# Kernel tuning notes

Hardware: AMD Instinct MI355X
Metric: run time of the kernel (lower is better)

Reference implementation:

```python
import jax, jax.numpy as jnp
import numpy as np

D_MODEL = 1024
N_HEADS = 16
HEAD_DIM = D_MODEL // N_HEADS
D_LATENT = 256
LAMBDA_DECAY = 0.01
TIME_STEP = 0.01  # get_timestamps spacing; wall-clock base cancels in diffs
CLAMP = 1e4


def setup_inputs() -> dict:
    key = jax.random.key(0)
    ks = jax.random.split(key, 8)
    B, S = 2, 2048
    def w(k, i, o):
        return jax.random.normal(k, (i, o), dtype=jnp.float32) * 0.02
    return {
        "x": jax.random.normal(ks[0], (B, S, D_MODEL), dtype=jnp.float32),
        "Wq": w(ks[1], D_MODEL, D_MODEL),
        "Wk": w(ks[2], D_MODEL, D_MODEL),
        "Wv": w(ks[3], D_MODEL, D_MODEL),
        "Wo": w(ks[4], D_MODEL, D_MODEL),
        "W_down_kv": w(ks[5], D_MODEL, D_LATENT),
        "W_up_k": w(ks[6], D_LATENT, D_MODEL),
        "W_up_v": w(ks[7], D_LATENT, D_MODEL),
    }


def reference(x, Wq, Wk, Wv, Wo, W_down_kv, W_up_k, W_up_v):
    B, S, _ = x.shape
    q = x @ Wq
    k = x @ Wk
    v = x @ Wv
    latent_kv = (k + v) @ W_down_kv            # [B,S,d_latent]
    k_rec = latent_kv @ W_up_k                 # [B,S,d_model]
    v_rec = latent_kv @ W_up_v
    # split heads -> [B,H,S,hd]
    def heads(t):
        return t.reshape(B, S, N_HEADS, HEAD_DIM).transpose(0, 2, 1, 3)
    qh, kh, vh = heads(q), heads(k_rec), heads(v_rec)
    scale = 1.0 / (jnp.sqrt(jnp.float32(D_MODEL)) + 1e-8)
    scores = jnp.einsum("bhqd,bhkd->bhqk", qh, kh) * scale
    scores = jnp.clip(jnp.nan_to_num(scores, nan=-1e9), -CLAMP, CLAMP)
    # time decay: |t_i - t_j| = TIME_STEP * |i - j| (wall-clock base cancels)
    idx = jnp.arange(S, dtype=jnp.float32)
    decay = jnp.exp(-LAMBDA_DECAY * TIME_STEP * jnp.abs(idx[:, None] - idx[None, :]))
    scores = scores * decay[None, None, :, :]
    scores = jnp.clip(jnp.nan_to_num(scores, nan=-1e9), -CLAMP, CLAMP)
    attn = jax.nn.softmax(scores, axis=-1)
    out = jnp.einsum("bhqk,bhkd->bhqd", attn, vh)
    out = out.transpose(0, 2, 1, 3).reshape(B, S, D_MODEL)
    return out @ Wo, latent_kv
```

## Files before the change

### kernel.cpp

```cpp
#include <hip/hip_runtime.h>
#include <hip/hip_bf16.h>
#include <cstdint>
#include <cstddef>

typedef __bf16 bf16;
typedef __bf16 bf16x8 __attribute__((ext_vector_type(8)));
typedef float f32x4 __attribute__((ext_vector_type(4)));

#define NB 2
#define SEQ 2048
#define DM 1024
#define MTOK 4096
#define DL 256
#define NH 16
#define HD 64

#define LOG2E 1.4426950408889634f

__device__ __forceinline__ void gload16(const void* g, void* l) {
  __builtin_amdgcn_global_load_lds((const __attribute__((address_space(1))) void*)g,
                                   (__attribute__((address_space(3))) void*)l, 16, 0, 0);
}
__device__ __forceinline__ float fast_exp2(float x) {
#if __has_builtin(__builtin_amdgcn_exp2f)
  return __builtin_amdgcn_exp2f(x);
#else
  float r; asm("v_exp_f32 %0, %1" : "=v"(r) : "v"(x)); return r;
#endif
}
__device__ __forceinline__ int xcd_swz(int orig, int nwg) {
  int x = orig & 7;
  int q = nwg >> 3, r = nwg & 7;
  int base = (x < r) ? x * (q + 1) : r * (q + 1) + (x - r) * q;
  return base + (orig >> 3);
}

__device__ __forceinline__ void transpose_dev(const float* __restrict__ in0,
                                              bf16* __restrict__ out, int R, int C,
                                              int c0, int r0, int tid, float (*tile)[33]) {
  int tx = tid & 31, ty = tid >> 5;
#pragma unroll
  for (int i = 0; i < 4; ++i) {
    int r = r0 + ty + 8 * i;
    tile[ty + 8 * i][tx] = in0[(size_t)r * C + c0 + tx];
  }
  __syncthreads();
  int c = tid >> 3, s = tid & 7;
  bf16 o4[4] __attribute__((aligned(8)));
#pragma unroll
  for (int j = 0; j < 4; ++j) o4[j] = (bf16)tile[4 * s + j][c];
  *reinterpret_cast<uint2*>(out + (size_t)(c0 + c) * R + r0 + 4 * s) =
      *reinterpret_cast<const uint2*>(o4);
}

__device__ __forceinline__ void cvt8_dev(const float* __restrict__ in, bf16* __restrict__ out,
                                         int blk, int tid) {
  int i = (blk * 256 + tid) * 8;
  float4 a = *reinterpret_cast<const float4*>(in + i);
  float4 b = *reinterpret_cast<const float4*>(in + i + 4);
  bf16 o[8] __attribute__((aligned(16)));
  o[0] = (bf16)a.x; o[1] = (bf16)a.y; o[2] = (bf16)a.z; o[3] = (bf16)a.w;
  o[4] = (bf16)b.x; o[5] = (bf16)b.y; o[6] = (bf16)b.z; o[7] = (bf16)b.w;
  *reinterpret_cast<uint4*>(out + i) = *reinterpret_cast<const uint4*>(o);
}

__device__ __forceinline__ void sum8_dev(const float* __restrict__ in0, const float* __restrict__ in1,
                                         bf16* __restrict__ out, int blk, int tid) {
  int i = (blk * 256 + tid) * 8;
  float4 a0 = *reinterpret_cast<const float4*>(in0 + i);
  float4 b0 = *reinterpret_cast<const float4*>(in0 + i + 4);
  float4 a1 = *reinterpret_cast<const float4*>(in1 + i);
  float4 b1 = *reinterpret_cast<const float4*>(in1 + i + 4);
  bf16 o[8] __attribute__((aligned(16)));
  o[0] = (bf16)(a0.x + a1.x); o[1] = (bf16)(a0.y + a1.y);
  o[2] = (bf16)(a0.z + a1.z); o[3] = (bf16)(a0.w + a1.w);
  o[4] = (bf16)(b0.x + b1.x); o[5] = (bf16)(b0.y + b1.y);
  o[6] = (bf16)(b0.z + b1.z); o[7] = (bf16)(b0.w + b1.w);
  *reinterpret_cast<uint4*>(out + i) = *reinterpret_cast<const uint4*>(o);
}

__global__ __launch_bounds__(256) void prep_kernel(const float* __restrict__ x,
                                                   const float* __restrict__ Wq,
                                                   const float* __restrict__ Wk,
                                                   const float* __restrict__ Wv,
                                                   const float* __restrict__ Wo,
                                                   const float* __restrict__ Wdn,
                                                   const float* __restrict__ Wuk,
                                                   const float* __restrict__ Wuv,
                                                   bf16* xbf, bf16* WqT, bf16* WoT, bf16* WdnT,
                                                   bf16* WukT, bf16* WuvT, bf16* Wkv) {
  __shared__ float tile[32][33];
  int id = blockIdx.x, tid = threadIdx.x;
  if (id < 2048) { cvt8_dev(x, xbf, id, tid); return; }
  id -= 2048;
  if (id < 512) { sum8_dev(Wk, Wv, Wkv, id, tid); return; }
  id -= 512;
  if (id < 1024) { transpose_dev(Wq, WqT, 1024, 1024, (id & 31) * 32, (id >> 5) * 32, tid, tile); return; }
  id -= 1024;
  if (id < 1024) { transpose_dev(Wo, WoT, 1024, 1024, (id & 31) * 32, (id >> 5) * 32, tid, tile); return; }
  id -= 1024;
  if (id < 256) { transpose_dev(Wdn, WdnT, 1024, 256, (id & 7) * 32, (id >> 3) * 32, tid, tile); return; }
  id -= 256;
  if (id < 256) { transpose_dev(Wuk, WukT, 256, 1024, (id & 31) * 32, (id >> 5) * 32, tid, tile); return; }
  id -= 256;
  transpose_dev(Wuv, WuvT, 256, 1024, (id & 31) * 32, (id >> 5) * 32, tid, tile);
}

template <int TN, int EPI>
__device__ __forceinline__ void gemm_core(const bf16* __restrict__ A, const bf16* __restrict__ Bt,
                                          bf16* __restrict__ O1, bf16* __restrict__ O2,
                                          float* __restrict__ Of,
                                          int K, int bx, int by, bf16* As, bf16* Bs) {
  const int tid = threadIdx.x;
  const int lane = tid & 63;
  const int wv = tid >> 6;
  const int wr = wv >> 1, wc = wv & 1;
  const int row0 = bx * 128, col0 = by * TN;
  const int l15 = lane & 15;
  const int kq = (lane >> 4) * 8;
  constexpr int NR = TN / 32;
  constexpr int BSZ = TN * 32;

  const bf16* aS = A + (size_t)(row0 + (tid >> 2)) * K + (tid & 3) * 8;
  const bf16* bS = Bt + (size_t)(col0 + (tid >> 2)) * K + (tid & 3) * 8;
  const int d0 = tid * 8, d1 = tid * 8 + 2048;

  gload16(aS, As + d0); gload16(aS + (size_t)64 * K, As + d1);
  gload16(bS, Bs + d0);
  if constexpr (TN == 128) gload16(bS + (size_t)64 * K, Bs + d1);
  aS += 32; bS += 32;

  f32x4 acc[4][NR] = {};
  int cur = 0;
  for (int k0 = 0; k0 < K; k0 += 32) {
    __syncthreads();
    if (k0 + 32 < K) {
      const int nxA = (cur ^ 1) * 4096, nxB = (cur ^ 1) * BSZ;
      gload16(aS, As + nxA + d0); gload16(aS + (size_t)64 * K, As + nxA + d1);
      gload16(bS, Bs + nxB + d0);
      if constexpr (TN == 128) gload16(bS + (size_t)64 * K, Bs + nxB + d1);
      aS += 32; bS += 32;
    }
    const bf16* Ab = As + cur * 4096;
    const bf16* Bb = Bs + cur * BSZ;
    bf16x8 af[4], bfr[NR];
#pragma unroll
    for (int m = 0; m < 4; ++m)
      af[m] = *reinterpret_cast<const bf16x8*>(&Ab[(wr * 64 + m * 16 + l15) * 32 + kq]);
#pragma unroll
    for (int n = 0; n < NR; ++n)
      bfr[n] = *reinterpret_cast<const bf16x8*>(&Bb[(wc * (TN / 2) + n * 16 + l15) * 32 + kq]);
    __builtin_amdgcn_s_setprio(1);
#pragma unroll
    for (int m = 0; m < 4; ++m)
#pragma unroll
      for (int n = 0; n < NR; ++n)
        acc[m][n] = __builtin_amdgcn_mfma_f32_16x16x32_bf16(af[m], bfr[n], acc[m][n], 0, 0, 0);
    __builtin_amdgcn_s_setprio(0);
    cur ^= 1;
  }

  const int rbase = row0 + wr * 64 + (lane >> 4) * 4;
  const int cbase = col0 + wc * (TN / 2) + l15;
#pragma unroll
  for (int m = 0; m < 4; ++m) {
#pragma unroll
    for (int n = 0; n < NR; ++n) {
      const int cc = cbase + n * 16;
      if constexpr (EPI == 0) {
#pragma unroll
        for (int r = 0; r < 4; ++r)
          O1[(size_t)(rbase + m * 16 + r) * DM + cc] = (bf16)acc[m][n][r];
      } else if constexpr (EPI == 3) {
#pragma unroll
        for (int r = 0; r < 4; ++r)
          Of[(size_t)(rbase + m * 16 + r) * DM + cc] = acc[m][n][r];
      } else if constexpr (EPI == 4) {
        if (cc < 1024) {
#pragma unroll
          for (int r = 0; r < 4; ++r)
            O1[(size_t)(rbase + m * 16 + r) * DM + cc] = (bf16)acc[m][n][r];
        } else {
          bf16 t4[4] __attribute__((aligned(8)));
#pragma unroll
          for (int r = 0; r < 4; ++r) t4[r] = (bf16)acc[m][n][r];
          *reinterpret_cast<uint2*>(O2 + (size_t)(cc - 1024) * MTOK + (rbase + m * 16)) =
              *reinterpret_cast<const uint2*>(t4);
        }
      } else {
#pragma unroll
        for (int r = 0; r < 4; ++r) {
          float v = acc[m][n][r];
          O1[(size_t)(rbase + m * 16 + r) * DL + cc] = (bf16)v;
          Of[(size_t)(rbase + m * 16 + r) * DL + cc] = v;
        }
      }
    }
  }
}

__global__ __launch_bounds__(256) void gemm_q_w(const bf16* __restrict__ xbf,
                                                const bf16* __restrict__ WqT, bf16* qbf,
                                                const bf16* __restrict__ WdnT,
                                                const bf16* __restrict__ Wkv, bf16* WkvdT) {
  __shared__ __align__(16) bf16 As[2 * 4096];
  __shared__ __align__(16) bf16 Bs[2 * 64 * 32];
  int id = xcd_swz(blockIdx.x, 544);
  if (id < 32)
    gemm_core<64, 0>(WdnT, Wkv, WkvdT, nullptr, nullptr, DM, id >> 4, id & 15, As, Bs);
  else {
    int j = id - 32;
    gemm_core<64, 0>(xbf, WqT, qbf, nullptr, nullptr, DM, j >> 4, j & 15, As, Bs);
  }
}

__global__ __launch_bounds__(256) void gemm_latent(const bf16* __restrict__ xbf,
                                                   const bf16* __restrict__ WkvdT,
                                                   bf16* latbf, float* out_lat) {
  __shared__ __align__(16) bf16 As[2 * 4096];
  __shared__ __align__(16) bf16 Bs[2 * 64 * 32];
  int id = xcd_swz(blockIdx.x, 128);
  gemm_core<64, 6>(xbf, WkvdT, latbf, nullptr, out_lat, DM, id >> 2, id & 3, As, Bs);
}

__global__ __launch_bounds__(256) void gemm_up(const bf16* __restrict__ latbf,
                                               const bf16* __restrict__ WupT,
                                               bf16* kbuf, bf16* vT) {
  __shared__ __align__(16) bf16 As[2 * 4096];
  __shared__ __align__(16) bf16 Bs[2 * 64 * 32];
  int id = xcd_swz(blockIdx.x, 1024);
  gemm_core<64, 4>(latbf, WupT, kbuf, vT, nullptr, DL, id >> 5, id & 31, As, Bs);
}

__global__ __launch_bounds__(256) void gemm_out(const bf16* __restrict__ ctx,
                                                const bf16* __restrict__ WoT, float* out0) {
  __shared__ __align__(16) bf16 As[2 * 4096];
  __shared__ __align__(16) bf16 Bs[2 * 64 * 32];
  int id = xcd_swz(blockIdx.x, 512);
  gemm_core<64, 3>(ctx, WoT, nullptr, nullptr, out0, DM, id >> 4, id & 15, As, Bs);
}

__global__ __launch_bounds__(256) void attn_kernel(const bf16* __restrict__ Q,
                                                   const bf16* __restrict__ Kr,
                                                   const bf16* __restrict__ Vt,
                                                   bf16* __restrict__ Ctx) {
  __shared__ __align__(16) bf16 Ks[2 * 4096];
  __shared__ __align__(16) bf16 Vs[2 * 4096];
  __shared__ __align__(16) bf16 Ps[4096];
  const int work = xcd_swz(blockIdx.x, SEQ / 64 * NH * NB);
  const int qt = work & 31, h = (work >> 5) & 15, b = work >> 9;
  const int tid = threadIdx.x, lane = tid & 63, wv = tid >> 6;
  const int l15 = lane & 15, lg = lane >> 4;
  const int qbase = qt * 64 + wv * 16;
  const size_t tok0 = (size_t)b * SEQ;

  bf16x8 qf[2];
  {
    const bf16* qp = Q + (tok0 + qbase + l15) * DM + h * HD + lg * 8;
    qf[0] = *reinterpret_cast<const bf16x8*>(qp);
    qf[1] = *reinterpret_cast<const bf16x8*>(qp + 32);
  }

  const int c1 = tid + 256;
  const int r0s = tid >> 3, r1s = c1 >> 3;
  const int cc0 = (tid & 7) ^ (r0s & 7), cc1 = (c1 & 7) ^ (r1s & 7);
  const bf16* kS0 = Kr + (tok0 + r0s) * DM + h * HD + cc0 * 8;
  const bf16* kS1 = Kr + (tok0 + r1s) * DM + h * HD + cc1 * 8;
  const bf16* vS0 = Vt + (size_t)(h * HD + r0s) * MTOK + tok0 + cc0 * 8;
  const bf16* vS1 = Vt + (size_t)(h * HD + r1s) * MTOK + tok0 + cc1 * 8;
  const int d0 = tid * 8, d1 = tid * 8 + 2048;

  gload16(kS0, Ks + d0); gload16(kS1, Ks + d1);
  gload16(vS0, Vs + d0); gload16(vS1, Vs + d1);
  kS0 += 64 * DM; kS1 += 64 * DM; vS0 += 64; vS1 += 64;

  int koff[2][4], poffw[4], poffr[2];
  const int hsw = l15 & 7;
#pragma unroll
  for (int ks = 0; ks < 2; ++ks)
#pragma unroll
    for (int nf = 0; nf < 4; ++nf) {
      int row = nf * 16 + l15;
      koff[ks][nf] = row * 64 + (((ks * 4 + lg) ^ (row & 7)) * 8);
    }
  const int psBase = wv * 1024 + l15 * 64;
#pragma unroll
  for (int nf = 0; nf < 4; ++nf)
    poffw[nf] = psBase + (((nf * 2 + (lg >> 1)) ^ hsw) * 8) + (lg & 1) * 4;
#pragma unroll
  for (int ks = 0; ks < 2; ++ks)
    poffr[ks] = psBase + (((ks * 4 + lg) ^ hsw) * 8);

  bf16x8 ones;
#pragma unroll
  for (int j = 0; j < 8; ++j) ones[j] = (bf16)1.0f;

  f32x4 oacc[4] = {};
  f32x4 lacc = {};
  float dec[4][4];
  const float DEC2C = (1.0f / 32.0f) * LOG2E;
  const float NC2 = -1.0e-4f * LOG2E;
  const float E64 = 0.99362048f, IE64 = 1.00642051f;
  const int ib = -qbase - l15 + lg * 4;

  int cur = 0;
  for (int t = 0; t < SEQ / 64; ++t) {
    const int key0 = t * 64;
    __syncthreads();
    if (t + 1 < SEQ / 64) {
      const int nx = (cur ^ 1) * 4096;
      gload16(kS0, Ks + nx + d0); gload16(kS1, Ks + nx + d1);
      gload16(vS0, Vs + nx + d0); gload16(vS1, Vs + nx + d1);
      kS0 += 64 * DM; kS1 += 64 * DM; vS0 += 64; vS1 += 64;
    }
    {
      bool before = (key0 + 63 < qbase);
      bool afterp = (key0 >= qbase + 79);
      if (t == 0 || (!before && !afterp)) {
#pragma unroll
        for (int nf = 0; nf < 4; ++nf)
#pragma unroll
          for (int r = 0; r < 4; ++r) {
            float df = (float)(key0 + ib + nf * 16 + r);
            dec[nf][r] = DEC2C * fast_exp2(NC2 * fabsf(df));
          }
      } else {
        float mlt = before ? IE64 : E64;
#pragma unroll
        for (int nf = 0; nf < 4; ++nf)
#pragma unroll
          for (int r = 0; r < 4; ++r) dec[nf][r] *= mlt;
      }
    }
    const int kb = cur * 4096;

    f32x4 sc[4] = {};
    __builtin_amdgcn_s_setprio(1);
#pragma unroll
    for (int ks = 0; ks < 2; ++ks)
#pragma unroll
      for (int nf = 0; nf < 4; ++nf) {
        bf16x8 kf = *reinterpret_cast<const bf16x8*>(&Ks[kb + koff[ks][nf]]);
        sc[nf] = __builtin_amdgcn_mfma_f32_16x16x32_bf16(kf, qf[ks], sc[nf], 0, 0, 0);
      }
    __builtin_amdgcn_s_setprio(0);

#pragma unroll
    for (int nf = 0; nf < 4; ++nf) {
      bf16 t4[4] __attribute__((aligned(8)));
#pragma unroll
      for (int r = 0; r < 4; ++r) t4[r] = (bf16)fast_exp2(sc[nf][r] * dec[nf][r]);
      *reinterpret_cast<uint2*>(&Ps[poffw[nf]]) = *reinterpret_cast<const uint2*>(t4);
    }
    bf16x8 pb[2];
    pb[0] = *reinterpret_cast<const bf16x8*>(&Ps[poffr[0]]);
    pb[1] = *reinterpret_cast<const bf16x8*>(&Ps[poffr[1]]);

    __builtin_amdgcn_s_setprio(1);
#pragma unroll
    for (int ks = 0; ks < 2; ++ks) {
#pragma unroll
      for (int nf = 0; nf < 4; ++nf) {
        bf16x8 vf = *reinterpret_cast<const bf16x8*>(&Vs[kb + koff[ks][nf]]);
        oacc[nf] = __builtin_amdgcn_mfma_f32_16x16x32_bf16(vf, pb[ks], oacc[nf], 0, 0, 0);
      }
      lacc = __builtin_amdgcn_mfma_f32_16x16x32_bf16(ones, pb[ks], lacc, 0, 0, 0);
    }
    __builtin_amdgcn_s_setprio(0);
    cur ^= 1;
  }

  const float inv = 1.0f / lacc[0];
#pragma unroll
  for (int nf = 0; nf < 4; ++nf) {
    bf16 o4[4] __attribute__((aligned(8)));
#pragma unroll
    for (int r = 0; r < 4; ++r) o4[r] = (bf16)(oacc[nf][r] * inv);
    *reinterpret_cast<uint2*>(Ctx + (tok0 + qbase + l15) * DM + h * HD + nf * 16 + lg * 4) =
        *reinterpret_cast<const uint2*>(o4);
  }
}

extern "C" void kernel_launch(void* const* d_in, const int* in_sizes, int n_in,
                              void* d_out, int out_size, void* d_ws, size_t ws_size,
                              hipStream_t stream) {
  const float* x   = (const float*)d_in[0];
  const float* Wq  = (const float*)d_in[1];
  const float* Wk  = (const float*)d_in[2];
  const float* Wv  = (const float*)d_in[3];
  const float* Wo  = (const float*)d_in[4];
  const float* Wdn = (const float*)d_in[5];
  const float* Wuk = (const float*)d_in[6];
  const float* Wuv = (const float*)d_in[7];
  float* out0 = (float*)d_out;
  float* out_lat = out0 + (size_t)MTOK * DM;

  char* ws = (char*)d_ws;
  const size_t MB = 1u << 20;
  bf16* xbf   = (bf16*)(ws + 0);
  bf16* qbf   = (bf16*)(ws + 8 * MB);
  bf16* kbuf  = (bf16*)(ws + 16 * MB);
  bf16* Wkv   = kbuf;
  bf16* WkvdT = (bf16*)(ws + 18 * MB);
  bf16* vT    = (bf16*)(ws + 24 * MB);
  bf16* latbf = (bf16*)(ws + 32 * MB);
  bf16* WqT   = (bf16*)(ws + 34 * MB);
  bf16* WoT   = (bf16*)(ws + 36 * MB);
  bf16* WukT  = (bf16*)(ws + 38 * MB);
  bf16* WuvT  = (bf16*)(ws + 38 * MB + 512 * 1024);
  bf16* WdnT  = (bf16*)(ws + 39 * MB);
  bf16* ctx   = xbf;

  prep_kernel<<<5376, 256, 0, stream>>>(x, Wq, Wk, Wv, Wo, Wdn, Wuk, Wuv,
                                        xbf, WqT, WoT, WdnT, WukT, WuvT, Wkv);
  gemm_q_w<<<544, 256, 0, stream>>>(xbf, WqT, qbf, WdnT, Wkv, WkvdT);
  gemm_latent<<<128, 256, 0, stream>>>(xbf, WkvdT, latbf, out_lat);
  gemm_up<<<1024, 256, 0, stream>>>(latbf, WukT, kbuf, vT);
  attn_kernel<<<1024, 256, 0, stream>>>(qbf, kbuf, vT, ctx);
  gemm_out<<<512, 256, 0, stream>>>(ctx, WoT, out0);

  (void)in_sizes; (void)n_in; (void)out_size; (void)ws_size;
}
```

Baseline: 136.9 us.

## Process two key tiles per iteration in attention with 128-key double buffer

The attention loop now stages 128 keys per iteration (two 64-key sub-tiles) in a larger double-buffered LDS region. This halves the number of __syncthreads barriers and gives the scheduler more independent MFMA and exp work to interleave. Both QK score sets are computed up front, and softmax of the second sub-tile overlaps with PV of the first using a separate P buffer. The cost is doubled LDS use (about 80KB per block), which may lower occupancy, plus higher register pressure from the two score accumulators.

```diff
diff --git a/kernel.cpp b/kernel.cpp
--- a/kernel.cpp
+++ b/kernel.cpp
@@ -244,9 +244,9 @@
                                                    const bf16* __restrict__ Kr,
                                                    const bf16* __restrict__ Vt,
                                                    bf16* __restrict__ Ctx) {
-  __shared__ __align__(16) bf16 Ks[2 * 4096];
-  __shared__ __align__(16) bf16 Vs[2 * 4096];
-  __shared__ __align__(16) bf16 Ps[4096];
+  __shared__ __align__(16) bf16 Ks[2 * 8192];
+  __shared__ __align__(16) bf16 Vs[2 * 8192];
+  __shared__ __align__(16) bf16 Ps[2 * 4096];
   const int work = xcd_swz(blockIdx.x, SEQ / 64 * NH * NB);
   const int qt = work & 31, h = (work >> 5) & 15, b = work >> 9;
   const int tid = threadIdx.x, lane = tid & 63, wv = tid >> 6;
@@ -271,8 +271,10 @@
   const int d0 = tid * 8, d1 = tid * 8 + 2048;
 
   gload16(kS0, Ks + d0); gload16(kS1, Ks + d1);
+  gload16(kS0 + 64 * DM, Ks + 4096 + d0); gload16(kS1 + 64 * DM, Ks + 4096 + d1);
   gload16(vS0, Vs + d0); gload16(vS1, Vs + d1);
-  kS0 += 64 * DM; kS1 += 64 * DM; vS0 += 64; vS1 += 64;
+  gload16(vS0 + 64, Vs + 4096 + d0); gload16(vS1 + 64, Vs + 4096 + d1);
+  kS0 += 128 * DM; kS1 += 128 * DM; vS0 += 128; vS1 += 128;
 
   int koff[2][4], poffw[4], poffr[2];
   const int hsw = l15 & 7;
@@ -303,45 +305,62 @@
   const float E64 = 0.99362048f, IE64 = 1.00642051f;
   const int ib = -qbase - l15 + lg * 4;
 
+#pragma unroll
+  for (int nf = 0; nf < 4; ++nf)
+#pragma unroll
+    for (int r = 0; r < 4; ++r) {
+      float df = (float)(ib + nf * 16 + r);
+      dec[nf][r] = DEC2C * fast_exp2(NC2 * fabsf(df));
+    }
+
+  auto upd_dec = [&](int key0) {
+    bool before = (key0 + 63 < qbase);
+    bool afterp = (key0 >= qbase + 79);
+    if (!before && !afterp) {
+#pragma unroll
+      for (int nf = 0; nf < 4; ++nf)
+#pragma unroll
+        for (int r = 0; r < 4; ++r) {
+          float df = (float)(key0 + ib + nf * 16 + r);
+          dec[nf][r] = DEC2C * fast_exp2(NC2 * fabsf(df));
+        }
+    } else {
+      float mlt = before ? IE64 : E64;
+#pragma unroll
+      for (int nf = 0; nf < 4; ++nf)
+#pragma unroll
+        for (int r = 0; r < 4; ++r) dec[nf][r] *= mlt;
+    }
+  };
+
   int cur = 0;
-  for (int t = 0; t < SEQ / 64; ++t) {
-    const int key0 = t * 64;
+  for (int tp = 0; tp < 16; ++tp) {
     __syncthreads();
-    if (t + 1 < SEQ / 64) {
-      const int nx = (cur ^ 1) * 4096;
+    if (tp + 1 < 16) {
+      const int nx = (cur ^ 1) * 8192;
       gload16(kS0, Ks + nx + d0); gload16(kS1, Ks + nx + d1);
+      gload16(kS0 + 64 * DM, Ks + nx + 4096 + d0); gload16(kS1 + 64 * DM, Ks + nx + 4096 + d1);
       gload16(vS0, Vs + nx + d0); gload16(vS1, Vs + nx + d1);
-      kS0 += 64 * DM; kS1 += 64 * DM; vS0 += 64; vS1 += 64;
-    }
-    {
-      bool before = (key0 + 63 < qbase);
-      bool afterp = (key0 >= qbase + 79);
-      if (t == 0 || (!before && !afterp)) {
-#pragma unroll
-        for (int nf = 0; nf < 4; ++nf)
-#pragma unroll
-          for (int r = 0; r < 4; ++r) {
-            float df = (float)(key0 + ib + nf * 16 + r);
-            dec[nf][r] = DEC2C * fast_exp2(NC2 * fabsf(df));
-          }
-      } else {
-        float mlt = before ? IE64 : E64;
-#pragma unroll
-        for (int nf = 0; nf < 4; ++nf)
-#pragma unroll
-          for (int r = 0; r < 4; ++r) dec[nf][r] *= mlt;
+      gload16(vS0 + 64, Vs + nx + 4096 + d0); gload16(vS1 + 64, Vs + nx + 4096 + d1);
+      kS0 += 128 * DM; kS1 += 128 * DM; vS0 += 128; vS1 += 128;
+    }
+    const int ka = cur * 8192;
+
+    f32x4 scA[4] = {}, scB[4] = {};
+    __builtin_amdgcn_s_setprio(1);
+#pragma unroll
+    for (int ks = 0; ks < 2; ++ks)
+#pragma unroll
+      for (int nf = 0; nf < 4; ++nf) {
+        bf16x8 kf = *reinterpret_cast<const bf16x8*>(&Ks[ka + koff[ks][nf]]);
+        scA[nf] = __builtin_amdgcn_mfma_f32_16x16x32_bf16(kf, qf[ks], scA[nf], 0, 0, 0);
       }
-    }
-    const int kb = cur * 4096;
-
-    f32x4 sc[4] = {};
-    __builtin_amdgcn_s_setprio(1);
 #pragma unroll
     for (int ks = 0; ks < 2; ++ks)
 #pragma unroll
       for (int nf = 0; nf < 4; ++nf) {
-        bf16x8 kf = *reinterpret_cast<const bf16x8*>(&Ks[kb + koff[ks][nf]]);
-        sc[nf] = __builtin_amdgcn_mfma_f32_16x16x32_bf16(kf, qf[ks], sc[nf], 0, 0, 0);
+        bf16x8 kf = *reinterpret_cast<const bf16x8*>(&Ks[ka + 4096 + koff[ks][nf]]);
+        scB[nf] = __builtin_amdgcn_mfma_f32_16x16x32_bf16(kf, qf[ks], scB[nf], 0, 0, 0);
       }
     __builtin_amdgcn_s_setprio(0);
 
@@ -349,24 +368,51 @@
     for (int nf = 0; nf < 4; ++nf) {
       bf16 t4[4] __attribute__((aligned(8)));
 #pragma unroll
-      for (int r = 0; r < 4; ++r) t4[r] = (bf16)fast_exp2(sc[nf][r] * dec[nf][r]);
+      for (int r = 0; r < 4; ++r) t4[r] = (bf16)fast_exp2(scA[nf][r] * dec[nf][r]);
       *reinterpret_cast<uint2*>(&Ps[poffw[nf]]) = *reinterpret_cast<const uint2*>(t4);
     }
+    bf16x8 pa[2];
+    pa[0] = *reinterpret_cast<const bf16x8*>(&Ps[poffr[0]]);
+    pa[1] = *reinterpret_cast<const bf16x8*>(&Ps[poffr[1]]);
+
+    upd_dec(tp * 128 + 64);
+
+    __builtin_amdgcn_s_setprio(1);
+#pragma unroll
+    for (int ks = 0; ks < 2; ++ks) {
+#pragma unroll
+      for (int nf = 0; nf < 4; ++nf) {
+        bf16x8 vf = *reinterpret_cast<const bf16x8*>(&Vs[ka + koff[ks][nf]]);
+        oacc[nf] = __builtin_amdgcn_mfma_f32_16x16x32_bf16(vf, pa[ks], oacc[nf], 0, 0, 0);
+      }
+      lacc = __builtin_amdgcn_mfma_f32_16x16x32_bf16(ones, pa[ks], lacc, 0, 0, 0);
+    }
+    __builtin_amdgcn_s_setprio(0);
+
+#pragma unroll
+    for (int nf = 0; nf < 4; ++nf) {
+      bf16 t4[4] __attribute__((aligned(8)));
+#pragma unroll
+      for (int r = 0; r < 4; ++r) t4[r] = (bf16)fast_exp2(scB[nf][r] * dec[nf][r]);
+      *reinterpret_cast<uint2*>(&Ps[4096 + poffw[nf]]) = *reinterpret_cast<const uint2*>(t4);
+    }
     bf16x8 pb[2];
-    pb[0] = *reinterpret_cast<const bf16x8*>(&Ps[poffr[0]]);
-    pb[1] = *reinterpret_cast<const bf16x8*>(&Ps[poffr[1]]);
+    pb[0] = *reinterpret_cast<const bf16x8*>(&Ps[4096 + poffr[0]]);
+    pb[1] = *reinterpret_cast<const bf16x8*>(&Ps[4096 + poffr[1]]);
 
     __builtin_amdgcn_s_setprio(1);
 #pragma unroll
     for (int ks = 0; ks < 2; ++ks) {
 #pragma unroll
       for (int nf = 0; nf < 4; ++nf) {
-        bf16x8 vf = *reinterpret_cast<const bf16x8*>(&Vs[kb + koff[ks][nf]]);
+        bf16x8 vf = *reinterpret_cast<const bf16x8*>(&Vs[ka + 4096 + koff[ks][nf]]);
         oacc[nf] = __builtin_amdgcn_mfma_f32_16x16x32_bf16(vf, pb[ks], oacc[nf], 0, 0, 0);
       }
       lacc = __builtin_amdgcn_mfma_f32_16x16x32_bf16(ones, pb[ks], lacc, 0, 0, 0);
     }
     __builtin_amdgcn_s_setprio(0);
+
+    if (tp + 1 < 16) upd_dec((tp + 1) * 128);
     cur ^= 1;
   }
 
```

After: 144.7 us. 1.06x slower.
